# Kernel tuning notes

Hardware: AMD Instinct MI355X
Metric: run time of the kernel (lower is better)

The kernel has to match this reference:

```python
import jax, jax.numpy as jnp
import numpy as np

B, T, D, U = 256, 2048, 64, 64


def setup_inputs() -> dict:
    key = jax.random.key(0)
    k1, k2, k3 = jax.random.split(key, 3)
    x = jax.random.normal(k1, (B, T, D), dtype=jnp.float32)
    Wx = jax.random.normal(k2, (D, 4 * U), dtype=jnp.float32) * 0.05
    Wh = jax.random.normal(k3, (U, 4 * U), dtype=jnp.float32) * 0.05
    b = jnp.zeros((4 * U,), dtype=jnp.float32)
    return {"x": x, "Wx": Wx, "Wh": Wh, "b": b}


def reference(x, Wx, Wh, b):
    # Keras LSTM gate order: i, f, g(candidate), o; act=tanh, rec_act=sigmoid.
    u = Wh.shape[0]
    # Precompute the input projection for all timesteps (same math, vectorized).
    xz = jnp.einsum('btd,dg->btg', x, Wx) + b  # [B, T, 4U]

    def step(carry, zt):
        h, c = carry                       # [B, U] each
        z = zt + h @ Wh                    # [B, 4U]
        i = jax.nn.sigmoid(z[:, :u])
        f = jax.nn.sigmoid(z[:, u:2 * u])
        g = jnp.tanh(z[:, 2 * u:3 * u])
        o = jax.nn.sigmoid(z[:, 3 * u:])
        c_new = f * c + i * g
        h_new = o * jnp.tanh(c_new)
        return (h_new, c_new), (c_new, h_new)

    h0 = jnp.zeros((x.shape[0], u), dtype=x.dtype)
    c0 = jnp.zeros((x.shape[0], u), dtype=x.dtype)
    _, (cs, hs) = jax.lax.scan(step, (h0, c0), jnp.swapaxes(xz, 0, 1))
    cs = jnp.swapaxes(cs, 0, 1)  # [B, T, U]
    hs = jnp.swapaxes(hs, 0, 1)  # [B, T, U]
    return jnp.concatenate([cs, hs], axis=-1)  # [B, T, 2U], cell states first
```

## Files before the change

### kernel.cpp

```cpp
#include <hip/hip_runtime.h>
#include <stdint.h>


#define T_STEPS 2048
#define DIM     64
#define GATES   256
#define CHUNK   16
#define NCHUNK  (T_STEPS / CHUNK)

typedef _Float16 f16;
typedef _Float16 f16x8 __attribute__((ext_vector_type(8)));
typedef float    f32x4 __attribute__((ext_vector_type(4)));

__device__ __forceinline__ void sync_lds() {
    __builtin_amdgcn_sched_barrier(0);
    asm volatile("s_waitcnt lgkmcnt(0)" ::: "memory");
    __builtin_amdgcn_sched_barrier(0);
    __builtin_amdgcn_s_barrier();
    __builtin_amdgcn_sched_barrier(0);
}

__device__ __forceinline__ float sigm(float z) {
    return __builtin_amdgcn_rcpf(1.f + __expf(-z));
}

#define MFMA16(A, B, C) __builtin_amdgcn_mfma_f32_16x16x32_f16(A, B, C, 0, 0, 0)

__device__ __forceinline__ void pack8(f16x8& d, const float4& a, const float4& b) {
    d[0]=(f16)a.x; d[1]=(f16)a.y; d[2]=(f16)a.z; d[3]=(f16)a.w;
    d[4]=(f16)b.x; d[5]=(f16)b.y; d[6]=(f16)b.z; d[7]=(f16)b.w;
}

__global__ __launch_bounds__(256, 1)
void lstm_r15_kernel(const float* __restrict__ x,
                     const float* __restrict__ Wx,
                     const float* __restrict__ Wh,
                     const float* __restrict__ bias,
                     float* __restrict__ out)
{
    __shared__ __align__(16) f16   sH[2][64];
    __shared__ __align__(16) float sXZ[4][CHUNK][16][4];

    const int tid  = threadIdx.x;
    const int lane = tid & 63;
    const int w    = tid >> 6;
    const int j    = lane & 15;
    const int g    = lane >> 4;
    const int u    = w * 16 + j;

    const int batch = blockIdx.x;
    const float* xb = x + (size_t)batch * T_STEPS * DIM;
    float* ob = out + (size_t)batch * T_STEPS * (2 * DIM);

    f16x8 Bh[4][2], Bx[4][2];
    f32x4 bias4[4];
#pragma unroll
    for (int q = 0; q < 4; ++q) {
        const int col = q * 64 + u;
        const float bb = bias[col];
        bias4[q][0] = bb; bias4[q][1] = bb; bias4[q][2] = bb; bias4[q][3] = bb;
#pragma unroll
        for (int ks = 0; ks < 2; ++ks)
#pragma unroll
            for (int e = 0; e < 8; ++e) {
                const int k = ks * 32 + g * 8 + e;
                Bh[q][ks][e] = (f16)Wh[k * GATES + col];
                Bx[q][ks][e] = (f16)Wx[k * GATES + col];
            }
    }
    const f32x4 zero4 = {0.f, 0.f, 0.f, 0.f};

    if (tid < 128) sH[tid >> 6][tid & 63] = (f16)0.f;

    float4 x0, x1, x2, x3;
    {
        const float* xr = xb + (size_t)j * DIM + g * 8;
        x0 = *(const float4*)(xr);      x1 = *(const float4*)(xr + 4);
        x2 = *(const float4*)(xr + 32); x3 = *(const float4*)(xr + 36);
    }

    float c = 0.f;
    __syncthreads();

#pragma unroll 1
    for (int n = 0; n < NCHUNK; ++n) {
        f16x8 ax0, ax1;
        pack8(ax0, x0, x1); pack8(ax1, x2, x3);
        f32x4 z0 = MFMA16(ax0, Bx[0][0], bias4[0]); z0 = MFMA16(ax1, Bx[0][1], z0);
        f32x4 z1 = MFMA16(ax0, Bx[1][0], bias4[1]); z1 = MFMA16(ax1, Bx[1][1], z1);
        f32x4 z2 = MFMA16(ax0, Bx[2][0], bias4[2]); z2 = MFMA16(ax1, Bx[2][1], z2);
        f32x4 z3 = MFMA16(ax0, Bx[3][0], bias4[3]); z3 = MFMA16(ax1, Bx[3][1], z3);
#pragma unroll
        for (int r = 0; r < 4; ++r) {
            float4 v = {z0[r], z1[r], z2[r], z3[r]};
            *(float4*)&sXZ[w][4 * g + r][j][0] = v;
        }
        float4 xzv = *(const float4*)&sXZ[w][0][j][0];

        if (n + 1 < NCHUNK) {
            const float* xr = xb + ((size_t)(n + 1) * CHUNK + j) * DIM + g * 8;
            x0 = *(const float4*)(xr);      x1 = *(const float4*)(xr + 4);
            x2 = *(const float4*)(xr + 32); x3 = *(const float4*)(xr + 36);
        }

        float* obn = ob + (size_t)n * CHUNK * 128;

#pragma unroll
        for (int s = 0; s < CHUNK; ++s) {
            const int pb = s & 1;
            f16x8 A0 = *(const f16x8*)&sH[pb][g * 8];
            f16x8 A1 = *(const f16x8*)&sH[pb][32 + g * 8];

            f32x4 h0 = MFMA16(A0, Bh[0][0], zero4); h0 = MFMA16(A1, Bh[0][1], h0);
            f32x4 h1 = MFMA16(A0, Bh[1][0], zero4); h1 = MFMA16(A1, Bh[1][1], h1);
            f32x4 h2 = MFMA16(A0, Bh[2][0], zero4); h2 = MFMA16(A1, Bh[2][1], h2);
            f32x4 h3 = MFMA16(A0, Bh[3][0], zero4); h3 = MFMA16(A1, Bh[3][1], h3);

            float zi = h0[0] + xzv.x, zf = h1[0] + xzv.y;
            float zg = h2[0] + xzv.z, zo = h3[0] + xzv.w;
            float gi = sigm(zi), gf = sigm(zf), go = sigm(zo);
            float gg = fmaf(2.f, sigm(zg + zg), -1.f);
            c = fmaf(gf, c, gi * gg);
            float e2 = __expf(-2.f * fabsf(c));
            float th = copysignf(
                fmaf(-2.f, e2 * __builtin_amdgcn_rcpf(1.f + e2), 1.f), c);
            float hh = go * th;

            float4 xzn = *(const float4*)&sXZ[w][(s + 1) & 15][j][0];

            if (g == 2)      sH[pb ^ 1][u] = (f16)hh;
            else if (g == 0) obn[s * 128 + u]      = c;
            else if (g == 1) obn[s * 128 + 64 + u] = hh;
            sync_lds();
            xzv = xzn;
        }
    }
}

extern "C" void kernel_launch(void* const* d_in, const int* in_sizes, int n_in,
                              void* d_out, int out_size, void* d_ws, size_t ws_size,
                              hipStream_t stream) {
    const float* x  = (const float*)d_in[0];
    const float* Wx = (const float*)d_in[1];
    const float* Wh = (const float*)d_in[2];
    const float* b  = (const float*)d_in[3];
    float* out = (float*)d_out;

    hipLaunchKernelGGL(lstm_r15_kernel, dim3(256), dim3(256), 0, stream,
                       x, Wx, Wh, b, out);
}
```

Measured before the change: 576.3 us.

## Split into producer and consumer waves, double-buffering the input projection

Doubles the block to 512 threads. Four producer waves compute the next chunk's input projection (x·Wx + bias) into a double-buffered LDS tile, spreading the loads, MFMAs and stores across the 16 recurrent steps. The four consumer waves only run the h·Wh recurrence and the gate math. This takes the per-chunk projection work off the serial critical path. In exchange, every step's barrier now covers 8 waves, and the x loads for chunk n+2 are issued while chunk n is being processed.

```diff
diff --git a/kernel.cpp b/kernel.cpp
--- a/kernel.cpp
+++ b/kernel.cpp
@@ -31,19 +31,21 @@
     d[4]=(f16)b.x; d[5]=(f16)b.y; d[6]=(f16)b.z; d[7]=(f16)b.w;
 }
 
-__global__ __launch_bounds__(256, 1)
-void lstm_r15_kernel(const float* __restrict__ x,
+__global__ __launch_bounds__(512, 1)
+void lstm_r17_kernel(const float* __restrict__ x,
                      const float* __restrict__ Wx,
                      const float* __restrict__ Wh,
                      const float* __restrict__ bias,
                      float* __restrict__ out)
 {
     __shared__ __align__(16) f16   sH[2][64];
-    __shared__ __align__(16) float sXZ[4][CHUNK][16][4];
+    __shared__ __align__(16) float sXZ[2][4][CHUNK][16][4];
 
     const int tid  = threadIdx.x;
     const int lane = tid & 63;
-    const int w    = tid >> 6;
+    const int wq   = tid >> 6;
+    const bool consumer = (wq < 4);
+    const int w    = wq & 3;
     const int j    = lane & 15;
     const int g    = lane >> 4;
     const int u    = w * 16 + j;
@@ -52,7 +54,8 @@
     const float* xb = x + (size_t)batch * T_STEPS * DIM;
     float* ob = out + (size_t)batch * T_STEPS * (2 * DIM);
 
-    f16x8 Bh[4][2], Bx[4][2];
+    const float* Wsrc = consumer ? Wh : Wx;
+    f16x8 Bw[4][2];
     f32x4 bias4[4];
 #pragma unroll
     for (int q = 0; q < 4; ++q) {
@@ -64,8 +67,7 @@
 #pragma unroll
             for (int e = 0; e < 8; ++e) {
                 const int k = ks * 32 + g * 8 + e;
-                Bh[q][ks][e] = (f16)Wh[k * GATES + col];
-                Bx[q][ks][e] = (f16)Wx[k * GATES + col];
+                Bw[q][ks][e] = (f16)Wsrc[k * GATES + col];
             }
     }
     const f32x4 zero4 = {0.f, 0.f, 0.f, 0.f};
@@ -73,66 +75,93 @@
     if (tid < 128) sH[tid >> 6][tid & 63] = (f16)0.f;
 
     float4 x0, x1, x2, x3;
-    {
+    f16x8 axc0, axc1;
+    f32x4 p0, p1, p2, p3;
+    if (!consumer) {
         const float* xr = xb + (size_t)j * DIM + g * 8;
         x0 = *(const float4*)(xr);      x1 = *(const float4*)(xr + 4);
         x2 = *(const float4*)(xr + 32); x3 = *(const float4*)(xr + 36);
+        pack8(axc0, x0, x1); pack8(axc1, x2, x3);
+        p0 = MFMA16(axc0, Bw[0][0], bias4[0]); p0 = MFMA16(axc1, Bw[0][1], p0);
+        p1 = MFMA16(axc0, Bw[1][0], bias4[1]); p1 = MFMA16(axc1, Bw[1][1], p1);
+        p2 = MFMA16(axc0, Bw[2][0], bias4[2]); p2 = MFMA16(axc1, Bw[2][1], p2);
+        p3 = MFMA16(axc0, Bw[3][0], bias4[3]); p3 = MFMA16(axc1, Bw[3][1], p3);
+#pragma unroll
+        for (int r = 0; r < 4; ++r) {
+            float4 v = {p0[r], p1[r], p2[r], p3[r]};
+            *(float4*)&sXZ[0][w][4 * g + r][j][0] = v;
+        }
+        const float* xr1 = xb + ((size_t)CHUNK + j) * DIM + g * 8;
+        x0 = *(const float4*)(xr1);      x1 = *(const float4*)(xr1 + 4);
+        x2 = *(const float4*)(xr1 + 32); x3 = *(const float4*)(xr1 + 36);
+        pack8(axc0, x0, x1); pack8(axc1, x2, x3);
     }
+    __syncthreads();
 
     float c = 0.f;
-    __syncthreads();
+    float4 xzv;
+    if (consumer) xzv = *(const float4*)&sXZ[0][w][0][j][0];
 
 #pragma unroll 1
     for (int n = 0; n < NCHUNK; ++n) {
-        f16x8 ax0, ax1;
-        pack8(ax0, x0, x1); pack8(ax1, x2, x3);
-        f32x4 z0 = MFMA16(ax0, Bx[0][0], bias4[0]); z0 = MFMA16(ax1, Bx[0][1], z0);
-        f32x4 z1 = MFMA16(ax0, Bx[1][0], bias4[1]); z1 = MFMA16(ax1, Bx[1][1], z1);
-        f32x4 z2 = MFMA16(ax0, Bx[2][0], bias4[2]); z2 = MFMA16(ax1, Bx[2][1], z2);
-        f32x4 z3 = MFMA16(ax0, Bx[3][0], bias4[3]); z3 = MFMA16(ax1, Bx[3][1], z3);
-#pragma unroll
-        for (int r = 0; r < 4; ++r) {
-            float4 v = {z0[r], z1[r], z2[r], z3[r]};
-            *(float4*)&sXZ[w][4 * g + r][j][0] = v;
-        }
-        float4 xzv = *(const float4*)&sXZ[w][0][j][0];
-
-        if (n + 1 < NCHUNK) {
-            const float* xr = xb + ((size_t)(n + 1) * CHUNK + j) * DIM + g * 8;
-            x0 = *(const float4*)(xr);      x1 = *(const float4*)(xr + 4);
-            x2 = *(const float4*)(xr + 32); x3 = *(const float4*)(xr + 36);
-        }
-
+        const int cb = n & 1, nb = cb ^ 1;
         float* obn = ob + (size_t)n * CHUNK * 128;
+        const bool mk1 = (n + 1 < NCHUNK);
+        const bool mk2 = (n + 2 < NCHUNK);
 
 #pragma unroll
         for (int s = 0; s < CHUNK; ++s) {
             const int pb = s & 1;
-            f16x8 A0 = *(const f16x8*)&sH[pb][g * 8];
-            f16x8 A1 = *(const f16x8*)&sH[pb][32 + g * 8];
+            if (consumer) {
+                f16x8 A0 = *(const f16x8*)&sH[pb][g * 8];
+                f16x8 A1 = *(const f16x8*)&sH[pb][32 + g * 8];
 
-            f32x4 h0 = MFMA16(A0, Bh[0][0], zero4); h0 = MFMA16(A1, Bh[0][1], h0);
-            f32x4 h1 = MFMA16(A0, Bh[1][0], zero4); h1 = MFMA16(A1, Bh[1][1], h1);
-            f32x4 h2 = MFMA16(A0, Bh[2][0], zero4); h2 = MFMA16(A1, Bh[2][1], h2);
-            f32x4 h3 = MFMA16(A0, Bh[3][0], zero4); h3 = MFMA16(A1, Bh[3][1], h3);
+                f32x4 h0 = MFMA16(A0, Bw[0][0], zero4); h0 = MFMA16(A1, Bw[0][1], h0);
+                f32x4 h1 = MFMA16(A0, Bw[1][0], zero4); h1 = MFMA16(A1, Bw[1][1], h1);
+                f32x4 h2 = MFMA16(A0, Bw[2][0], zero4); h2 = MFMA16(A1, Bw[2][1], h2);
+                f32x4 h3 = MFMA16(A0, Bw[3][0], zero4); h3 = MFMA16(A1, Bw[3][1], h3);
 
-            float zi = h0[0] + xzv.x, zf = h1[0] + xzv.y;
-            float zg = h2[0] + xzv.z, zo = h3[0] + xzv.w;
-            float gi = sigm(zi), gf = sigm(zf), go = sigm(zo);
-            float gg = fmaf(2.f, sigm(zg + zg), -1.f);
-            c = fmaf(gf, c, gi * gg);
-            float e2 = __expf(-2.f * fabsf(c));
-            float th = copysignf(
-                fmaf(-2.f, e2 * __builtin_amdgcn_rcpf(1.f + e2), 1.f), c);
-            float hh = go * th;
+                float zi = h0[0] + xzv.x, zf = h1[0] + xzv.y;
+                float zg = h2[0] + xzv.z, zo = h3[0] + xzv.w;
+                float gi = sigm(zi), gf = sigm(zf), go = sigm(zo);
+                float gg = fmaf(2.f, sigm(zg + zg), -1.f);
+                c = fmaf(gf, c, gi * gg);
+                float e2 = __expf(-2.f * fabsf(c));
+                float th = copysignf(
+                    fmaf(-2.f, e2 * __builtin_amdgcn_rcpf(1.f + e2), 1.f), c);
+                float hh = go * th;
 
-            float4 xzn = *(const float4*)&sXZ[w][(s + 1) & 15][j][0];
+                float4 xzn = (s == 15)
+                    ? *(const float4*)&sXZ[nb][w][0][j][0]
+                    : *(const float4*)&sXZ[cb][w][s + 1][j][0];
 
-            if (g == 2)      sH[pb ^ 1][u] = (f16)hh;
-            else if (g == 0) obn[s * 128 + u]      = c;
-            else if (g == 1) obn[s * 128 + 64 + u] = hh;
+                if (g == 2)      sH[pb ^ 1][u] = (f16)hh;
+                else if (g == 0) obn[s * 128 + u]      = c;
+                else if (g == 1) obn[s * 128 + 64 + u] = hh;
+                xzv = xzn;
+            } else {
+                if (mk1) {
+                    if (s == 0) { p0 = MFMA16(axc0, Bw[0][0], bias4[0]); p0 = MFMA16(axc1, Bw[0][1], p0); }
+                    if (s == 1) { p1 = MFMA16(axc0, Bw[1][0], bias4[1]); p1 = MFMA16(axc1, Bw[1][1], p1); }
+                    if (s == 2) { p2 = MFMA16(axc0, Bw[2][0], bias4[2]); p2 = MFMA16(axc1, Bw[2][1], p2); }
+                    if (s == 3) { p3 = MFMA16(axc0, Bw[3][0], bias4[3]); p3 = MFMA16(axc1, Bw[3][1], p3); }
+                    if (s >= 4 && s < 8) {
+                        const int r = s - 4;
+                        float4 v = {p0[r], p1[r], p2[r], p3[r]};
+                        *(float4*)&sXZ[nb][w][4 * g + r][j][0] = v;
+                    }
+                }
+                if (mk2) {
+                    const float* xr = xb + ((size_t)(n + 2) * CHUNK + j) * DIM + g * 8;
+                    if (s == 8)  x0 = *(const float4*)(xr);
+                    if (s == 9)  x1 = *(const float4*)(xr + 4);
+                    if (s == 10) x2 = *(const float4*)(xr + 32);
+                    if (s == 11) x3 = *(const float4*)(xr + 36);
+                    if (s == 12) pack8(axc0, x0, x1);
+                    if (s == 13) pack8(axc1, x2, x3);
+                }
+            }
             sync_lds();
-            xzv = xzn;
         }
     }
 }
@@ -146,6 +175,6 @@
     const float* b  = (const float*)d_in[3];
     float* out = (float*)d_out;
 
-    hipLaunchKernelGGL(lstm_r15_kernel, dim3(256), dim3(256), 0, stream,
+    hipLaunchKernelGGL(lstm_r17_kernel, dim3(256), dim3(512), 0, stream,
                        x, Wx, Wh, b, out);
 }
```

After: 595.6 us. +3.3%, slower.
